# Kernel optimization log

Measured on AMD Instinct MI355X. Metric: run time of the kernel, lower is better.

The kernel has to match this reference:

```python
import jax, jax.numpy as jnp
import numpy as np

NEG = -1e30

def setup_inputs() -> dict:
    key = jax.random.key(0)
    k1, k2, k3, k4, k5, k6, k7, k8 = jax.random.split(key, 8)
    B, Ti, Tm = 4, 512, 1024
    Din, Dmem, D = 256, 256, 64
    inputs = jax.random.normal(k1, (B, Ti, Din), dtype=jnp.float32)
    memory = jax.random.normal(k2, (B, Tm, Dmem), dtype=jnp.float32)
    input_lengths = jax.random.randint(k3, (B,), 1, Ti + 1)
    memory_lengths = jax.random.randint(k4, (B,), 1, Tm + 1)
    s_in = 1.0 / np.sqrt(Din)
    s_d = 1.0 / np.sqrt(D)
    W_in = jax.random.uniform(k5, (D, Din), jnp.float32, -s_in, s_in)
    b_in = jax.random.uniform(k6, (D,), jnp.float32, -s_in, s_in)
    W_mem = jax.random.uniform(k7, (D, Dmem), jnp.float32, -s_in, s_in)
    W_final = jax.random.uniform(k8, (D,), jnp.float32, -s_d, s_d)
    return {"inputs": inputs, "memory": memory,
            "input_lengths": input_lengths, "memory_lengths": memory_lengths,
            "W_in": W_in, "b_in": b_in, "W_mem": W_mem, "W_final": W_final}

def reference(inputs, memory, input_lengths, memory_lengths, W_in, b_in, W_mem, W_final):
    # inputs: (B,Ti,Din), memory: (B,Tm,Dmem)
    input_item = jnp.einsum('bid,td->bit', inputs, W_in) + b_in      # (B,Ti,D)
    memory_item = jnp.einsum('bmd,td->bmt', memory, W_mem)           # (B,Tm,D)
    items = jnp.tanh(input_item[:, :, None, :] + memory_item[:, None, :, :])  # (B,Ti,Tm,D)
    score = jnp.einsum('bitd,d->bit'.replace('t', 'mt')[:0] or 'bimd,d->bim', items, W_final)  # (B,Ti,Tm)
    Ti = inputs.shape[-2]
    Tm = memory.shape[-2]
    in_mask = jnp.arange(Ti)[None, :] < input_lengths[:, None]       # (B,Ti)
    mem_mask = jnp.arange(Tm)[None, :] < memory_lengths[:, None]     # (B,Tm)
    score = jnp.where(in_mask[:, :, None], score, NEG)
    score = jnp.where(mem_mask[:, None, :], score, NEG)
    attn = jax.nn.softmax(score, axis=-1)                            # (B,Ti,Tm)
    out = jnp.einsum('bim,bmd->bid', attn, memory)                   # (B,Ti,Dmem)
    return out
```

## Files before the change

### kernel.cpp

```cpp
#include <hip/hip_runtime.h>

#define C2  2.8853900817779268f
#define L2E 1.4426950408889634f

typedef float float2v __attribute__((ext_vector_type(2)));

__device__ __forceinline__ float2v pk_fma(float2v a, float2v b, float2v c) {
  float2v d;
  asm("v_pk_fma_f32 %0, %1, %2, %3" : "=v"(d) : "v"(a), "v"(b), "v"(c));
  return d;
}
__device__ __forceinline__ float2v pk_fma_bl(float2v a, float2v b, float2v c) {
  float2v d;
  asm("v_pk_fma_f32 %0, %1, %2, %3 op_sel:[0,0,0] op_sel_hi:[1,0,1]"
      : "=v"(d) : "v"(a), "v"(b), "v"(c));
  return d;
}
__device__ __forceinline__ float2v pk_fma_bh(float2v a, float2v b, float2v c) {
  float2v d;
  asm("v_pk_fma_f32 %0, %1, %2, %3 op_sel:[0,1,0] op_sel_hi:[1,1,1]"
      : "=v"(d) : "v"(a), "v"(b), "v"(c));
  return d;
}

__global__ __launch_bounds__(256) void proj_kernel(
    const float* __restrict__ inputs, const float* __restrict__ memory,
    const float* __restrict__ W_in, const float* __restrict__ b_in,
    const float* __restrict__ W_mem,
    float* __restrict__ in_item, float* __restrict__ mem_itemT)
{
  const int NIN = 2048;
  int blk = blockIdx.x;
  int dg = blk & 3;
  int r0 = (blk >> 2) * 16;
  int tid = threadIdx.x;
  int dl = tid & 15;
  int rw = tid >> 4;
  int d  = dg * 16 + dl;

  __shared__ float4 wlds[16][64];

  bool is_in = (r0 < NIN);
  const float* Wsel  = is_in ? W_in  : W_mem;
  const float* Abase = is_in ? inputs : memory;
  int ar0 = is_in ? r0 : r0 - NIN;

  const float4* Wv = reinterpret_cast<const float4*>(Wsel + (size_t)dg * 16 * 256);
  #pragma unroll
  for (int u = 0; u < 4; ++u) {
    int e = tid + u * 256;
    int j = e >> 6, k4 = e & 63;
    wlds[j][k4 ^ (j & 7)] = Wv[e];
  }
  float bias = is_in ? b_in[d] : 0.f;
  __syncthreads();

  const float4* A0 = reinterpret_cast<const float4*>(Abase + (size_t)(ar0 + rw) * 256);
  float2v acc = {0.f, 0.f};
  #pragma unroll 8
  for (int k4 = 0; k4 < 64; ++k4) {
    float4 w = wlds[dl][k4 ^ (dl & 7)];
    float4 a = A0[k4];
    acc = pk_fma(float2v{a.x, a.y}, float2v{w.x, w.y}, acc);
    acc = pk_fma(float2v{a.z, a.w}, float2v{w.z, w.w}, acc);
  }
  float val = (acc.x + acc.y + bias) * C2;
  int row = ar0 + rw;
  if (is_in) {
    in_item[(size_t)row * 64 + d] = val;
  } else {
    int b_ = row >> 10, m = row & 1023;
    mem_itemT[((size_t)(b_ * 16 + (d >> 2)) * 1024 + m) * 4 + (d & 3)] = val;
  }
}

__global__ __launch_bounds__(512, 4) void attn_kernel(
    const float* __restrict__ in_item,
    const float* __restrict__ mem_itemT,
    const float* __restrict__ memory,
    const int* __restrict__ in_len, const int* __restrict__ mem_len,
    const float* __restrict__ W_final,
    float* __restrict__ o_part,
    float* __restrict__ psum_part,
    int m_count)
{
  const int Ti = 512, Tm = 1024, DM = 256;
  const int TI = 4, MT = 128;
  const int NT = m_count >> 7;
  int lin = blockIdx.x;
  int b, z, it;
  if (m_count == 512) { b = lin & 3; z = (lin >> 2) & 1; it = lin >> 3; }
  else                { b = lin & 3; z = 0;              it = lin >> 2; }
  int i0 = it * TI;
  int m_begin = z * m_count;
  int tid = threadIdx.x;

  __shared__ float4 mt[2][16 * 128];
  __shared__ float4 pt4[2][128];
  __shared__ float  red[8];

  const int s_ii = __builtin_amdgcn_readfirstlane(tid >> 7);
  const int s_ml = tid & 127;
  const int dq = tid & 63, wv_ = tid >> 6;

  float4 qreg[16];
  {
    const float4* qrow = reinterpret_cast<const float4*>(
        in_item + ((size_t)b * Ti + i0 + s_ii) * 64);
    #pragma unroll
    for (int j = 0; j < 16; ++j) qreg[j] = qrow[j];
  }

  float Wsum = 0.f;
  #pragma unroll
  for (int j = 0; j < 64; ++j) Wsum += W_final[j];
  const float c1 = L2E * Wsum;
  const float4* Wf4 = reinterpret_cast<const float4*>(W_final);

  int ilen = in_len[b], mlen = mem_len[b];
  const bool row_valid = (i0 + s_ii) < ilen;

  const float4* mT4 = reinterpret_cast<const float4*>(mem_itemT);
  const int bb16 = b * 16;
  const float* memb = memory + (size_t)b * Tm * DM;

  float psum = 0.f;
  float2v a0x = {0,0}, a0z = {0,0}, a1x = {0,0}, a1z = {0,0};
  float2v a2x = {0,0}, a2z = {0,0}, a3x = {0,0}, a3z = {0,0};

  #pragma unroll
  for (int u = 0; u < 4; ++u) {
    int e = tid + u * 512;
    int dd4 = e >> 7, mm = e & 127;
    float4 v = mT4[(size_t)(bb16 + dd4) * 1024 + m_begin + mm];
    mt[0][dd4 * 128 + (mm ^ (dd4 & 7))] = v;
  }
  __syncthreads();

  #pragma unroll 1
  for (int t = 0; t < NT; ++t) {
    int m0 = m_begin + t * MT;
    int cur = t & 1;

    float4 stg0, stg1, stg2, stg3;
    bool do_stage = (t + 1 < NT);
    if (do_stage) {
      int m0n = m0 + MT;
      int e0 = tid, e1 = tid + 512, e2 = tid + 1024, e3 = tid + 1536;
      stg0 = mT4[(size_t)(bb16 + (e0 >> 7)) * 1024 + m0n + (e0 & 127)];
      stg1 = mT4[(size_t)(bb16 + (e1 >> 7)) * 1024 + m0n + (e1 & 127)];
      stg2 = mT4[(size_t)(bb16 + (e2 >> 7)) * 1024 + m0n + (e2 & 127)];
      stg3 = mT4[(size_t)(bb16 + (e3 >> 7)) * 1024 + m0n + (e3 & 127)];
    }

    {
      float4 S4 = make_float4(0.f, 0.f, 0.f, 0.f);
      #pragma unroll
      for (int d4 = 0; d4 < 16; ++d4) {
        float4 mv = mt[cur][d4 * 128 + (s_ml ^ (d4 & 7))];
        float4 qv = qreg[d4];
        float4 w  = Wf4[d4];
        S4.x = fmaf(w.x, __builtin_amdgcn_rcpf(1.0f + __builtin_amdgcn_exp2f(qv.x + mv.x)), S4.x);
        S4.y = fmaf(w.y, __builtin_amdgcn_rcpf(1.0f + __builtin_amdgcn_exp2f(qv.y + mv.y)), S4.y);
        S4.z = fmaf(w.z, __builtin_amdgcn_rcpf(1.0f + __builtin_amdgcn_exp2f(qv.z + mv.z)), S4.z);
        S4.w = fmaf(w.w, __builtin_amdgcn_rcpf(1.0f + __builtin_amdgcn_exp2f(qv.w + mv.w)), S4.w);
      }
      float S = (S4.x + S4.y) + (S4.z + S4.w);
      int mi = m0 + s_ml;
      float p = row_valid ? ((mi < mlen) ? __builtin_amdgcn_exp2f(fmaf(-C2, S, c1)) : 0.f)
                          : 1.0f;
      reinterpret_cast<float*>(&pt4[cur][s_ml])[s_ii] = p;
      psum += p;
    }

    if (do_stage) {
      int nxt = cur ^ 1;
      int e0 = tid, e1 = tid + 512, e2 = tid + 1024, e3 = tid + 1536;
      mt[nxt][(e0 >> 7) * 128 + ((e0 & 127) ^ ((e0 >> 7) & 7))] = stg0;
      mt[nxt][(e1 >> 7) * 128 + ((e1 & 127) ^ ((e1 >> 7) & 7))] = stg1;
      mt[nxt][(e2 >> 7) * 128 + ((e2 & 127) ^ ((e2 >> 7) & 7))] = stg2;
      mt[nxt][(e3 >> 7) * 128 + ((e3 & 127) ^ ((e3 >> 7) & 7))] = stg3;
    }
    __syncthreads();

    {
      const float* mpb = memb + (size_t)(m0 + wv_ * 16) * DM + dq * 4;
      #pragma unroll
      for (int mm = 0; mm < 16; ++mm) {
        float4 v  = *reinterpret_cast<const float4*>(mpb + (size_t)mm * DM);
        float4 pp = pt4[cur][wv_ * 16 + mm];
        float2v vx = {v.x, v.y}, vz = {v.z, v.w};
        float2v pxy = {pp.x, pp.y}, pzw = {pp.z, pp.w};
        a0x = pk_fma_bl(vx, pxy, a0x);  a0z = pk_fma_bl(vz, pxy, a0z);
        a1x = pk_fma_bh(vx, pxy, a1x);  a1z = pk_fma_bh(vz, pxy, a1z);
        a2x = pk_fma_bl(vx, pzw, a2x);  a2z = pk_fma_bl(vz, pzw, a2z);
        a3x = pk_fma_bh(vx, pzw, a3x);  a3z = pk_fma_bh(vz, pzw, a3z);
      }
    }
  }

  {
    float s = psum;
    #pragma unroll
    for (int o = 32; o >= 1; o >>= 1) s += __shfl_xor(s, o);
    if (dq == 0) red[wv_] = s;
  }
  float4* osl = &mt[0][0];
  osl[(wv_ * 4 + 0) * 64 + dq] = make_float4(a0x.x, a0x.y, a0z.x, a0z.y);
  osl[(wv_ * 4 + 1) * 64 + dq] = make_float4(a1x.x, a1x.y, a1z.x, a1z.y);
  osl[(wv_ * 4 + 2) * 64 + dq] = make_float4(a2x.x, a2x.y, a2z.x, a2z.y);
  osl[(wv_ * 4 + 3) * 64 + dq] = make_float4(a3x.x, a3x.y, a3z.x, a3z.y);
  __syncthreads();

  if (tid < 256) {
    int ii = tid >> 6, d2 = tid & 63;
    float4 s = osl[ii * 64 + d2];
    #pragma unroll
    for (int w = 1; w < 8; ++w) {
      float4 v = osl[(w * 4 + ii) * 64 + d2];
      s.x += v.x; s.y += v.y; s.z += v.z; s.w += v.w;
    }
    size_t r = (size_t)b * Ti + i0 + ii;
    reinterpret_cast<float4*>(o_part)[((size_t)z * 2048 + r) * 64 + d2] = s;
  }
  if (tid < TI) {
    psum_part[(size_t)z * 2048 + (size_t)b * Ti + i0 + tid] = red[2 * tid] + red[2 * tid + 1];
  }
}

__global__ __launch_bounds__(256) void combine_kernel(
    const float* __restrict__ o_part, const float* __restrict__ psum_part,
    float* __restrict__ out, int nsplit)
{
  int e = blockIdx.x * 256 + threadIdx.x;
  int r = e >> 6;
  const float4* op4 = reinterpret_cast<const float4*>(o_part);
  float4 o = op4[e];
  float s = psum_part[r];
  if (nsplit == 2) {
    float4 o1 = op4[e + 131072];
    o.x += o1.x; o.y += o1.y; o.z += o1.z; o.w += o1.w;
    s += psum_part[r + 2048];
  }
  float inv = __builtin_amdgcn_rcpf(s);
  o.x *= inv; o.y *= inv; o.z *= inv; o.w *= inv;
  reinterpret_cast<float4*>(out)[e] = o;
}

extern "C" void kernel_launch(void* const* d_in, const int* in_sizes, int n_in,
                              void* d_out, int out_size, void* d_ws, size_t ws_size,
                              hipStream_t stream) {
  const float* inputs   = (const float*)d_in[0];
  const float* memory   = (const float*)d_in[1];
  const int*   in_len   = (const int*)  d_in[2];
  const int*   mem_len  = (const int*)  d_in[3];
  const float* W_in     = (const float*)d_in[4];
  const float* b_in     = (const float*)d_in[5];
  const float* W_mem    = (const float*)d_in[6];
  const float* W_final  = (const float*)d_in[7];
  float* out = (float*)d_out;

  float* in_item   = (float*)d_ws;
  float* mem_itemT = in_item + 2048 * 64;
  float* o_part    = mem_itemT + 4096 * 64;
  float* psum_part = o_part + 2 * 2048 * 256;

  size_t need2 = (size_t)(131072 + 262144 + 2 * 524288 + 2 * 2048 + 64) * 4;
  int nsplit = (ws_size >= need2) ? 2 : 1;

  proj_kernel<<<1536, 256, 0, stream>>>(inputs, memory, W_in, b_in, W_mem,
                                        in_item, mem_itemT);
  attn_kernel<<<dim3(512 * nsplit), 512, 0, stream>>>(
      in_item, mem_itemT, memory, in_len, mem_len, W_final,
      o_part, psum_part, 1024 / nsplit);
  combine_kernel<<<512, 256, 0, stream>>>(o_part, psum_part, out, nsplit);
}
```

Before: 85.34 us.

## Halve attention block to 256 threads with 64-wide memory tiles

Shrinks the attention kernel block from 512 to 256 threads and the memory tile from 128 to 64 positions, so each block iterates over twice as many tiles. The memory-item LDS tile drops from double to single buffering, which adds a second barrier per iteration. Smaller blocks and less LDS are meant to allow more resident blocks per CU and better latency hiding. The cost is twice as many iterations and barriers, plus a shorter final reduction over 4 waves instead of 8.

```diff
diff --git a/kernel.cpp b/kernel.cpp
--- a/kernel.cpp
+++ b/kernel.cpp
@@ -74,7 +74,7 @@
   }
 }
 
-__global__ __launch_bounds__(512, 4) void attn_kernel(
+__global__ __launch_bounds__(256, 8) void attn_kernel(
     const float* __restrict__ in_item,
     const float* __restrict__ mem_itemT,
     const float* __restrict__ memory,
@@ -85,8 +85,8 @@
     int m_count)
 {
   const int Ti = 512, Tm = 1024, DM = 256;
-  const int TI = 4, MT = 128;
-  const int NT = m_count >> 7;
+  const int TI = 4, MT = 64;
+  const int NT = m_count >> 6;
   int lin = blockIdx.x;
   int b, z, it;
   if (m_count == 512) { b = lin & 3; z = (lin >> 2) & 1; it = lin >> 3; }
@@ -95,12 +95,12 @@
   int m_begin = z * m_count;
   int tid = threadIdx.x;
 
-  __shared__ float4 mt[2][16 * 128];
-  __shared__ float4 pt4[2][128];
-  __shared__ float  red[8];
-
-  const int s_ii = __builtin_amdgcn_readfirstlane(tid >> 7);
-  const int s_ml = tid & 127;
+  __shared__ float4 mt[16 * 64];
+  __shared__ float4 pt4[2][64];
+  __shared__ float  red[4];
+
+  const int s_ii = __builtin_amdgcn_readfirstlane(tid >> 6);
+  const int s_ml = tid & 63;
   const int dq = tid & 63, wv_ = tid >> 6;
 
   float4 qreg[16];
@@ -130,34 +130,32 @@
 
   #pragma unroll
   for (int u = 0; u < 4; ++u) {
-    int e = tid + u * 512;
-    int dd4 = e >> 7, mm = e & 127;
-    float4 v = mT4[(size_t)(bb16 + dd4) * 1024 + m_begin + mm];
-    mt[0][dd4 * 128 + (mm ^ (dd4 & 7))] = v;
+    int e = tid + u * 256;
+    int d4 = e >> 6, mm = e & 63;
+    mt[d4 * 64 + (mm ^ (d4 & 7))] = mT4[(size_t)(bb16 + d4) * 1024 + m_begin + mm];
   }
   __syncthreads();
 
   #pragma unroll 1
   for (int t = 0; t < NT; ++t) {
     int m0 = m_begin + t * MT;
-    int cur = t & 1;
 
     float4 stg0, stg1, stg2, stg3;
     bool do_stage = (t + 1 < NT);
     if (do_stage) {
-      int m0n = m0 + MT;
-      int e0 = tid, e1 = tid + 512, e2 = tid + 1024, e3 = tid + 1536;
-      stg0 = mT4[(size_t)(bb16 + (e0 >> 7)) * 1024 + m0n + (e0 & 127)];
-      stg1 = mT4[(size_t)(bb16 + (e1 >> 7)) * 1024 + m0n + (e1 & 127)];
-      stg2 = mT4[(size_t)(bb16 + (e2 >> 7)) * 1024 + m0n + (e2 & 127)];
-      stg3 = mT4[(size_t)(bb16 + (e3 >> 7)) * 1024 + m0n + (e3 & 127)];
+      int m0n = m0 + MT - m_begin;
+      int e0 = tid, e1 = tid + 256, e2 = tid + 512, e3 = tid + 768;
+      stg0 = mT4[(size_t)(bb16 + (e0 >> 6)) * 1024 + m_begin + m0n + (e0 & 63)];
+      stg1 = mT4[(size_t)(bb16 + (e1 >> 6)) * 1024 + m_begin + m0n + (e1 & 63)];
+      stg2 = mT4[(size_t)(bb16 + (e2 >> 6)) * 1024 + m_begin + m0n + (e2 & 63)];
+      stg3 = mT4[(size_t)(bb16 + (e3 >> 6)) * 1024 + m_begin + m0n + (e3 & 63)];
     }
 
     {
       float4 S4 = make_float4(0.f, 0.f, 0.f, 0.f);
       #pragma unroll
       for (int d4 = 0; d4 < 16; ++d4) {
-        float4 mv = mt[cur][d4 * 128 + (s_ml ^ (d4 & 7))];
+        float4 mv = mt[d4 * 64 + (s_ml ^ (d4 & 7))];
         float4 qv = qreg[d4];
         float4 w  = Wf4[d4];
         S4.x = fmaf(w.x, __builtin_amdgcn_rcpf(1.0f + __builtin_amdgcn_exp2f(qv.x + mv.x)), S4.x);
@@ -169,26 +167,25 @@
       int mi = m0 + s_ml;
       float p = row_valid ? ((mi < mlen) ? __builtin_amdgcn_exp2f(fmaf(-C2, S, c1)) : 0.f)
                           : 1.0f;
-      reinterpret_cast<float*>(&pt4[cur][s_ml])[s_ii] = p;
+      reinterpret_cast<float*>(&pt4[t & 1][s_ml])[s_ii] = p;
       psum += p;
     }
+    __syncthreads();
 
     if (do_stage) {
-      int nxt = cur ^ 1;
-      int e0 = tid, e1 = tid + 512, e2 = tid + 1024, e3 = tid + 1536;
-      mt[nxt][(e0 >> 7) * 128 + ((e0 & 127) ^ ((e0 >> 7) & 7))] = stg0;
-      mt[nxt][(e1 >> 7) * 128 + ((e1 & 127) ^ ((e1 >> 7) & 7))] = stg1;
-      mt[nxt][(e2 >> 7) * 128 + ((e2 & 127) ^ ((e2 >> 7) & 7))] = stg2;
-      mt[nxt][(e3 >> 7) * 128 + ((e3 & 127) ^ ((e3 >> 7) & 7))] = stg3;
-    }
-    __syncthreads();
+      int e0 = tid, e1 = tid + 256, e2 = tid + 512, e3 = tid + 768;
+      mt[(e0 >> 6) * 64 + ((e0 & 63) ^ ((e0 >> 6) & 7))] = stg0;
+      mt[(e1 >> 6) * 64 + ((e1 & 63) ^ ((e1 >> 6) & 7))] = stg1;
+      mt[(e2 >> 6) * 64 + ((e2 & 63) ^ ((e2 >> 6) & 7))] = stg2;
+      mt[(e3 >> 6) * 64 + ((e3 & 63) ^ ((e3 >> 6) & 7))] = stg3;
+    }
 
     {
       const float* mpb = memb + (size_t)(m0 + wv_ * 16) * DM + dq * 4;
       #pragma unroll
       for (int mm = 0; mm < 16; ++mm) {
         float4 v  = *reinterpret_cast<const float4*>(mpb + (size_t)mm * DM);
-        float4 pp = pt4[cur][wv_ * 16 + mm];
+        float4 pp = pt4[t & 1][wv_ * 16 + mm];
         float2v vx = {v.x, v.y}, vz = {v.z, v.w};
         float2v pxy = {pp.x, pp.y}, pzw = {pp.z, pp.w};
         a0x = pk_fma_bl(vx, pxy, a0x);  a0z = pk_fma_bl(vz, pxy, a0z);
@@ -197,6 +194,7 @@
         a3x = pk_fma_bh(vx, pzw, a3x);  a3z = pk_fma_bh(vz, pzw, a3z);
       }
     }
+    __syncthreads();
   }
 
   {
@@ -205,18 +203,18 @@
     for (int o = 32; o >= 1; o >>= 1) s += __shfl_xor(s, o);
     if (dq == 0) red[wv_] = s;
   }
-  float4* osl = &mt[0][0];
+  float4* osl = &mt[0];
   osl[(wv_ * 4 + 0) * 64 + dq] = make_float4(a0x.x, a0x.y, a0z.x, a0z.y);
   osl[(wv_ * 4 + 1) * 64 + dq] = make_float4(a1x.x, a1x.y, a1z.x, a1z.y);
   osl[(wv_ * 4 + 2) * 64 + dq] = make_float4(a2x.x, a2x.y, a2z.x, a2z.y);
   osl[(wv_ * 4 + 3) * 64 + dq] = make_float4(a3x.x, a3x.y, a3z.x, a3z.y);
   __syncthreads();
 
-  if (tid < 256) {
+  {
     int ii = tid >> 6, d2 = tid & 63;
     float4 s = osl[ii * 64 + d2];
     #pragma unroll
-    for (int w = 1; w < 8; ++w) {
+    for (int w = 1; w < 4; ++w) {
       float4 v = osl[(w * 4 + ii) * 64 + d2];
       s.x += v.x; s.y += v.y; s.z += v.z; s.w += v.w;
     }
@@ -224,7 +222,7 @@
     reinterpret_cast<float4*>(o_part)[((size_t)z * 2048 + r) * 64 + d2] = s;
   }
   if (tid < TI) {
-    psum_part[(size_t)z * 2048 + (size_t)b * Ti + i0 + tid] = red[2 * tid] + red[2 * tid + 1];
+    psum_part[(size_t)z * 2048 + (size_t)b * Ti + i0 + tid] = red[tid];
   }
 }
 
@@ -270,7 +268,7 @@
 
   proj_kernel<<<1536, 256, 0, stream>>>(inputs, memory, W_in, b_in, W_mem,
                                         in_item, mem_itemT);
-  attn_kernel<<<dim3(512 * nsplit), 512, 0, stream>>>(
+  attn_kernel<<<dim3(512 * nsplit), 256, 0, stream>>>(
       in_item, mem_itemT, memory, in_len, mem_len, W_final,
       o_part, psum_part, 1024 / nsplit);
   combine_kernel<<<512, 256, 0, stream>>>(o_part, psum_part, out, nsplit);
```

After: 125.3 us. 46.9% more time.
